# Optimization experiments

Hardware: AMD Instinct MI355X
Metric: run time of the kernel (lower is better)

Reference implementation:

```python
import jax, jax.numpy as jnp
import numpy as np

B, D, HID = 32768, 5, 128
MU, SIGMA = 0.05, 0.2
T_MAX = 1.0


def setup_inputs() -> dict:
    key = jax.random.key(0)
    ks = jax.random.split(key, 5)
    t = T_MAX * jax.random.uniform(ks[0], (B, 1), jnp.float32)          # t in [t0, T]
    x = 0.5 + 2.0 * jax.random.uniform(ks[1], (B, D), jnp.float32)      # domain sampling as in fit()
    Win = jax.random.normal(ks[2], (D + 1, HID), jnp.float32) / np.float32(np.sqrt(D + 1))
    b_in = jnp.zeros((HID,), jnp.float32)
    # 3 DGM layers x 4 gates (Z, G, R, H), each Linear(d+1+HID, HID)
    Wg = jax.random.normal(ks[3], (3, 4, D + 1 + HID, HID), jnp.float32) / np.float32(np.sqrt(D + 1 + HID))
    bg = jnp.zeros((3, 4, HID), jnp.float32)
    Wout = jax.random.normal(ks[4], (HID, 1), jnp.float32) / np.float32(np.sqrt(HID))
    bout = jnp.zeros((1,), jnp.float32)
    return {"t": t, "x": x, "Win": Win, "b_in": b_in, "Wg": Wg, "bg": bg,
            "Wout": Wout, "bout": bout}


def _net(Win, b_in, Wg, bg, Wout, bout, t, x):
    """Net_DGM forward: input layer + 3 gated DGM layers + output layer. u: [B,1]."""
    tx = jnp.concatenate([t, x], axis=1)                 # [B, D+1]
    S = jnp.tanh(tx @ Win + b_in)                        # [B, HID]
    for i in range(3):                                   # fixed small layer loop
        xS = jnp.concatenate([tx, S], axis=1)            # [B, D+1+HID]
        Z = jnp.tanh(xS @ Wg[i, 0] + bg[i, 0])
        G = jnp.tanh(xS @ Wg[i, 1] + bg[i, 1])
        R = jnp.tanh(xS @ Wg[i, 2] + bg[i, 2])
        H = jnp.tanh(jnp.concatenate([tx, S * R], axis=1) @ Wg[i, 3] + bg[i, 3])
        S = (1.0 - G) * H + Z * S
    return S @ Wout + bout                               # [B, 1]


def reference(t, x, Win, b_in, Wg, bg, Wout, bout):
    """Black-Scholes PDE residual: u_t + mu*x.grad_x(u) + 0.5*sigma^2*Lap(u) - mu*u."""
    def u_sum(tt, xx):
        return _net(Win, b_in, Wg, bg, Wout, bout, tt, xx).sum()

    u = _net(Win, b_in, Wg, bg, Wout, bout, t, x)        # [B,1]
    grad_t, grad_x = jax.grad(u_sum, argnums=(0, 1))(t, x)  # [B,1], [B,D]

    # Hessian diagonal via forward-over-reverse (replaces torch's per-dim grad loop)
    gx = lambda xx: jax.grad(u_sum, argnums=1)(t, xx)    # [B,D] -> [B,D]

    def hvp(e):                                          # e: [D] unit vector
        return jax.jvp(gx, (x,), (jnp.broadcast_to(e, x.shape),))[1]  # [B,D]

    Hd = jax.vmap(hvp)(jnp.eye(D, dtype=x.dtype))        # [D, B, D]
    lap = jnp.einsum('ibi->b', Hd)[:, None]              # sum of Hessian diagonal, [B,1]

    drift = jnp.sum(MU * jax.lax.stop_gradient(x) * grad_x, axis=1, keepdims=True)
    pde = grad_t + drift + 0.5 * SIGMA ** 2 * lap - MU * u
    return pde
```

## Files before the change

### kernel.cpp

```cpp
#include <hip/hip_runtime.h>
#include <math.h>


namespace {
constexpr int HID_  = 128;
constexpr int NCH   = 12;
constexpr int ASTR  = 16;
constexpr int SPB   = 4;
constexpr float MU_   = 0.05f;
constexpr float HSIG2 = 0.5f * 0.2f * 0.2f;
}

__global__ __launch_bounds__(64 * SPB, 3)
void dgm_pde(const float* __restrict__ t,
             const float* __restrict__ x,
             const float* __restrict__ Win,
             const float* __restrict__ b_in,
             const float* __restrict__ Wg,
             const float* __restrict__ bg,
             const float* __restrict__ Wout,
             const float* __restrict__ bout,
             float* __restrict__ out)
{
    __shared__ __align__(16) float Abuf[SPB][HID_][ASTR];
    const int wv = threadIdx.x >> 6;
    const int l  = threadIdx.x & 63;
    const int samp = blockIdx.x * SPB + wv;
    float (*A)[ASTR] = Abuf[wv];
    const int j0 = 2 * l;

    float tx[6];
    tx[0] = t[samp];
    #pragma unroll
    for (int m = 1; m < 6; ++m) tx[m] = x[samp * 5 + m - 1];

    float S0[NCH], S1[NCH];
    {
        float w0[6], w1[6];
        #pragma unroll
        for (int m = 0; m < 6; ++m) {
            const float2 ww = *reinterpret_cast<const float2*>(Win + m * HID_ + j0);
            w0[m] = ww.x; w1[m] = ww.y;
        }
        const float2 bb = *reinterpret_cast<const float2*>(b_in + j0);
        float p0 = bb.x, p1 = bb.y;
        #pragma unroll
        for (int m = 0; m < 6; ++m) { p0 = fmaf(tx[m], w0[m], p0); p1 = fmaf(tx[m], w1[m], p1); }
        const float v0 = tanhf(p0), v1 = tanhf(p1);
        const float t20 = 1.f - v0 * v0, t21 = 1.f - v1 * v1;
        S0[0] = v0; S1[0] = v1;
        #pragma unroll
        for (int m = 0; m < 6; ++m) { S0[1 + m] = t20 * w0[m]; S1[1 + m] = t21 * w1[m]; }
        #pragma unroll
        for (int k = 1; k <= 5; ++k) {
            S0[6 + k] = -2.f * v0 * t20 * w0[k] * w0[k];
            S1[6 + k] = -2.f * v1 * t21 * w1[k] * w1[k];
        }
    }

    auto storeA = [&](const float* a0, const float* a1) {
        #pragma unroll
        for (int c = 0; c < NCH; c += 4) {
            *reinterpret_cast<float4*>(&A[j0][c])     = make_float4(a0[c], a0[c+1], a0[c+2], a0[c+3]);
            *reinterpret_cast<float4*>(&A[j0 + 1][c]) = make_float4(a1[c], a1[c+1], a1[c+2], a1[c+3]);
        }
    };
    auto matmul = [&](const float* __restrict__ Wgt, const float* __restrict__ bgt,
                      float* acc0, float* acc1) {
        #pragma unroll
        for (int c = 0; c < NCH; ++c) { acc0[c] = 0.f; acc1[c] = 0.f; }
        const float2 bb = *reinterpret_cast<const float2*>(bgt + j0);
        acc0[0] = bb.x; acc1[0] = bb.y;
        #pragma unroll
        for (int m = 0; m < 6; ++m) {
            const float2 w = *reinterpret_cast<const float2*>(Wgt + m * HID_ + j0);
            acc0[0] = fmaf(tx[m], w.x, acc0[0]);
            acc1[0] = fmaf(tx[m], w.y, acc1[0]);
            acc0[1 + m] += w.x;
            acc1[1 + m] += w.y;
        }
        #pragma unroll 2
        for (int h = 0; h < HID_; ++h) {
            const float2 w = *reinterpret_cast<const float2*>(Wgt + (6 + h) * HID_ + j0);
            const float4* A4 = reinterpret_cast<const float4*>(A[h]);
            const float4 a0 = A4[0], a1 = A4[1], a2 = A4[2];
            const float av[12] = {a0.x, a0.y, a0.z, a0.w,
                                  a1.x, a1.y, a1.z, a1.w,
                                  a2.x, a2.y, a2.z, a2.w};
            #pragma unroll
            for (int c = 0; c < NCH; ++c) {
                acc0[c] = fmaf(av[c], w.x, acc0[c]);
                acc1[c] = fmaf(av[c], w.y, acc1[c]);
            }
        }
    };
    auto act = [&](float* a) {
        const float v  = tanhf(a[0]);
        const float t2 = 1.f - v * v;
        #pragma unroll
        for (int k = 1; k <= 5; ++k) a[6 + k] = t2 * a[6 + k] - 2.f * v * t2 * a[1 + k] * a[1 + k];
        #pragma unroll
        for (int m = 0; m < 6; ++m) a[1 + m] = t2 * a[1 + m];
        a[0] = v;
    };

    storeA(S0, S1);
    __syncthreads();

    float Z0[NCH], Z1[NCH], G0[NCH], G1[NCH], R0[NCH], R1[NCH];
    constexpr int GSTride = 134 * HID_;
    #pragma unroll 1
    for (int layer = 0; layer < 3; ++layer) {
        const float* WL = Wg + (size_t)layer * 4 * GSTride;
        const float* bL = bg + layer * 4 * HID_;

        matmul(WL + 0 * GSTride, bL + 0 * HID_, Z0, Z1); act(Z0); act(Z1);
        matmul(WL + 1 * GSTride, bL + 1 * HID_, G0, G1); act(G0); act(G1);
        matmul(WL + 2 * GSTride, bL + 2 * HID_, R0, R1); act(R0); act(R1);

        #pragma unroll
        for (int k = 1; k <= 5; ++k) {
            R0[6+k] = S0[6+k]*R0[0] + 2.f*S0[1+k]*R0[1+k] + S0[0]*R0[6+k];
            R1[6+k] = S1[6+k]*R1[0] + 2.f*S1[1+k]*R1[1+k] + S1[0]*R1[6+k];
        }
        #pragma unroll
        for (int m = 0; m < 6; ++m) {
            R0[1+m] = S0[1+m]*R0[0] + S0[0]*R0[1+m];
            R1[1+m] = S1[1+m]*R1[0] + S1[0]*R1[1+m];
        }
        R0[0] = S0[0]*R0[0];
        R1[0] = S1[0]*R1[0];

        __syncthreads();
        storeA(R0, R1);
        __syncthreads();

        matmul(WL + 3 * GSTride, bL + 3 * HID_, R0, R1); act(R0); act(R1);

        #pragma unroll
        for (int k = 1; k <= 5; ++k) {
            S0[6+k] = (1.f - G0[0])*R0[6+k] - G0[6+k]*R0[0] - 2.f*G0[1+k]*R0[1+k]
                    + Z0[6+k]*S0[0] + 2.f*Z0[1+k]*S0[1+k] + Z0[0]*S0[6+k];
            S1[6+k] = (1.f - G1[0])*R1[6+k] - G1[6+k]*R1[0] - 2.f*G1[1+k]*R1[1+k]
                    + Z1[6+k]*S1[0] + 2.f*Z1[1+k]*S1[1+k] + Z1[0]*S1[6+k];
        }
        #pragma unroll
        for (int m = 0; m < 6; ++m) {
            S0[1+m] = (1.f - G0[0])*R0[1+m] - G0[1+m]*R0[0] + Z0[1+m]*S0[0] + Z0[0]*S0[1+m];
            S1[1+m] = (1.f - G1[0])*R1[1+m] - G1[1+m]*R1[0] + Z1[1+m]*S1[0] + Z1[0]*S1[1+m];
        }
        S0[0] = (1.f - G0[0])*R0[0] + Z0[0]*S0[0];
        S1[0] = (1.f - G1[0])*R1[0] + Z1[0]*S1[0];

        __syncthreads();
        storeA(S0, S1);
        __syncthreads();
    }

    float comb0 = S0[1] - MU_ * S0[0];
    float comb1 = S1[1] - MU_ * S1[0];
    #pragma unroll
    for (int k = 1; k <= 5; ++k) {
        comb0 += MU_ * tx[k] * S0[1 + k] + HSIG2 * S0[6 + k];
        comb1 += MU_ * tx[k] * S1[1 + k] + HSIG2 * S1[6 + k];
    }
    const float2 wo = *reinterpret_cast<const float2*>(Wout + j0);
    float part = comb0 * wo.x + comb1 * wo.y;
    #pragma unroll
    for (int off = 32; off > 0; off >>= 1) part += __shfl_xor(part, off, 64);
    if (l == 0) out[samp] = part - MU_ * bout[0];
}

extern "C" void kernel_launch(void* const* d_in, const int* in_sizes, int n_in,
                              void* d_out, int out_size, void* d_ws, size_t ws_size,
                              hipStream_t stream)
{
    const float* t    = (const float*)d_in[0];
    const float* x    = (const float*)d_in[1];
    const float* Win  = (const float*)d_in[2];
    const float* b_in = (const float*)d_in[3];
    const float* Wg   = (const float*)d_in[4];
    const float* bg   = (const float*)d_in[5];
    const float* Wout = (const float*)d_in[6];
    const float* bout = (const float*)d_in[7];
    float* out = (float*)d_out;

    const int nB = in_sizes[0];
    dgm_pde<<<nB / SPB, 64 * SPB, 0, stream>>>(t, x, Win, b_in, Wg, bg, Wout, bout, out);
}
```

Baseline: 2.680 ms.

## Use one-wave blocks, double-buffer S/P tiles, reorder gates and software-pipeline the matmul loads

Switches from four samples per 256-thread block to one sample per 64-thread block, with separate shared buffers for S and S*R. Gate evaluation is reordered so Z and G no longer need to live across the H matmul, which cuts register pressure. The inner matmul is hand software-pipelined, prefetching LDS rows and weight pairs two steps ahead. The intent is to hide load latency and raise occupancy, at the cost of more blocks and per-block overhead.

```diff
diff --git a/kernel.cpp b/kernel.cpp
--- a/kernel.cpp
+++ b/kernel.cpp
@@ -3,15 +3,36 @@
 
 
 namespace {
-constexpr int HID_  = 128;
-constexpr int NCH   = 12;
-constexpr int ASTR  = 16;
-constexpr int SPB   = 4;
+constexpr int HID_ = 128;
+constexpr int NCH  = 12;
+constexpr int ASTR = 16;
 constexpr float MU_   = 0.05f;
 constexpr float HSIG2 = 0.5f * 0.2f * 0.2f;
 }
 
-__global__ __launch_bounds__(64 * SPB, 3)
+#define LOADA(AB, h, A0, A1, A2) do {                                     \
+    const float4* _A4 = reinterpret_cast<const float4*>((AB)[(h)]);       \
+    A0 = _A4[0]; A1 = _A4[1]; A2 = _A4[2]; } while (0)
+
+#define LOADW(h, Wv) do {                                                 \
+    Wv = *reinterpret_cast<const float2*>(Wb + (size_t)(h) * HID_); } while (0)
+
+#define FMA12(A0, A1, A2, Wv) do {                                        \
+    acc0[0]  = fmaf((A0).x, (Wv).x, acc0[0]);  acc1[0]  = fmaf((A0).x, (Wv).y, acc1[0]);  \
+    acc0[1]  = fmaf((A0).y, (Wv).x, acc0[1]);  acc1[1]  = fmaf((A0).y, (Wv).y, acc1[1]);  \
+    acc0[2]  = fmaf((A0).z, (Wv).x, acc0[2]);  acc1[2]  = fmaf((A0).z, (Wv).y, acc1[2]);  \
+    acc0[3]  = fmaf((A0).w, (Wv).x, acc0[3]);  acc1[3]  = fmaf((A0).w, (Wv).y, acc1[3]);  \
+    acc0[4]  = fmaf((A1).x, (Wv).x, acc0[4]);  acc1[4]  = fmaf((A1).x, (Wv).y, acc1[4]);  \
+    acc0[5]  = fmaf((A1).y, (Wv).x, acc0[5]);  acc1[5]  = fmaf((A1).y, (Wv).y, acc1[5]);  \
+    acc0[6]  = fmaf((A1).z, (Wv).x, acc0[6]);  acc1[6]  = fmaf((A1).z, (Wv).y, acc1[6]);  \
+    acc0[7]  = fmaf((A1).w, (Wv).x, acc0[7]);  acc1[7]  = fmaf((A1).w, (Wv).y, acc1[7]);  \
+    acc0[8]  = fmaf((A2).x, (Wv).x, acc0[8]);  acc1[8]  = fmaf((A2).x, (Wv).y, acc1[8]);  \
+    acc0[9]  = fmaf((A2).y, (Wv).x, acc0[9]);  acc1[9]  = fmaf((A2).y, (Wv).y, acc1[9]);  \
+    acc0[10] = fmaf((A2).z, (Wv).x, acc0[10]); acc1[10] = fmaf((A2).z, (Wv).y, acc1[10]); \
+    acc0[11] = fmaf((A2).w, (Wv).x, acc0[11]); acc1[11] = fmaf((A2).w, (Wv).y, acc1[11]); \
+} while (0)
+
+__global__ __launch_bounds__(64, 3)
 void dgm_pde(const float* __restrict__ t,
              const float* __restrict__ x,
              const float* __restrict__ Win,
@@ -22,12 +43,11 @@
              const float* __restrict__ bout,
              float* __restrict__ out)
 {
-    __shared__ __align__(16) float Abuf[SPB][HID_][ASTR];
-    const int wv = threadIdx.x >> 6;
-    const int l  = threadIdx.x & 63;
-    const int samp = blockIdx.x * SPB + wv;
-    float (*A)[ASTR] = Abuf[wv];
-    const int j0 = 2 * l;
+    __shared__ __align__(16) float A_S[HID_][ASTR];
+    __shared__ __align__(16) float A_P[HID_][ASTR];
+    const int l    = threadIdx.x;
+    const int samp = blockIdx.x;
+    const int j0   = 2 * l;
 
     float tx[6];
     tx[0] = t[samp];
@@ -58,41 +78,55 @@
         }
     }
 
-    auto storeA = [&](const float* a0, const float* a1) {
+    auto storeJ = [&](float (*AB)[ASTR], const float* a0, const float* a1) {
         #pragma unroll
         for (int c = 0; c < NCH; c += 4) {
-            *reinterpret_cast<float4*>(&A[j0][c])     = make_float4(a0[c], a0[c+1], a0[c+2], a0[c+3]);
-            *reinterpret_cast<float4*>(&A[j0 + 1][c]) = make_float4(a1[c], a1[c+1], a1[c+2], a1[c+3]);
-        }
-    };
-    auto matmul = [&](const float* __restrict__ Wgt, const float* __restrict__ bgt,
-                      float* acc0, float* acc1) {
-        #pragma unroll
-        for (int c = 0; c < NCH; ++c) { acc0[c] = 0.f; acc1[c] = 0.f; }
-        const float2 bb = *reinterpret_cast<const float2*>(bgt + j0);
-        acc0[0] = bb.x; acc1[0] = bb.y;
+            *reinterpret_cast<float4*>(&AB[j0][c])     = make_float4(a0[c], a0[c+1], a0[c+2], a0[c+3]);
+            *reinterpret_cast<float4*>(&AB[j0 + 1][c]) = make_float4(a1[c], a1[c+1], a1[c+2], a1[c+3]);
+        }
+    };
+    auto matmul = [&](const float (*Ab)[ASTR],
+                      const float* __restrict__ Wgt, const float* __restrict__ bgt,
+                      float* __restrict__ acc0, float* __restrict__ acc1) {
+        #pragma unroll
+        for (int c = 1; c < NCH; ++c) { acc0[c] = 0.f; acc1[c] = 0.f; }
+        {
+            const float2 bb = *reinterpret_cast<const float2*>(bgt + j0);
+            acc0[0] = bb.x; acc1[0] = bb.y;
+        }
         #pragma unroll
         for (int m = 0; m < 6; ++m) {
-            const float2 w = *reinterpret_cast<const float2*>(Wgt + m * HID_ + j0);
-            acc0[0] = fmaf(tx[m], w.x, acc0[0]);
-            acc1[0] = fmaf(tx[m], w.y, acc1[0]);
-            acc0[1 + m] += w.x;
-            acc1[1 + m] += w.y;
-        }
-        #pragma unroll 2
-        for (int h = 0; h < HID_; ++h) {
-            const float2 w = *reinterpret_cast<const float2*>(Wgt + (6 + h) * HID_ + j0);
-            const float4* A4 = reinterpret_cast<const float4*>(A[h]);
-            const float4 a0 = A4[0], a1 = A4[1], a2 = A4[2];
-            const float av[12] = {a0.x, a0.y, a0.z, a0.w,
-                                  a1.x, a1.y, a1.z, a1.w,
-                                  a2.x, a2.y, a2.z, a2.w};
-            #pragma unroll
-            for (int c = 0; c < NCH; ++c) {
-                acc0[c] = fmaf(av[c], w.x, acc0[c]);
-                acc1[c] = fmaf(av[c], w.y, acc1[c]);
-            }
-        }
+            const float2 wh = *reinterpret_cast<const float2*>(Wgt + m * HID_ + j0);
+            acc0[0] = fmaf(tx[m], wh.x, acc0[0]);
+            acc1[0] = fmaf(tx[m], wh.y, acc1[0]);
+            acc0[1 + m] += wh.x; acc1[1 + m] += wh.y;
+        }
+        const float* Wb = Wgt + 6 * HID_ + j0;
+        float4 pa0, pa1, pa2, qa0, qa1, qa2;
+        float2 wr0, wr1, wr2, wr3;
+        LOADW(0, wr0); LOADW(1, wr1); LOADW(2, wr2); LOADW(3, wr3);
+        LOADA(Ab, 0, pa0, pa1, pa2);
+        LOADA(Ab, 1, qa0, qa1, qa2);
+        #pragma unroll 4
+        for (int h = 0; h + 5 < HID_; h += 2) {
+            float4 na0, na1, na2, ma0, ma1, ma2;
+            float2 t0, t1;
+            LOADA(Ab, h + 2, na0, na1, na2);
+            LOADA(Ab, h + 3, ma0, ma1, ma2);
+            LOADW(h + 4, t0); LOADW(h + 5, t1);
+            FMA12(pa0, pa1, pa2, wr0);
+            FMA12(qa0, qa1, qa2, wr1);
+            pa0 = na0; pa1 = na1; pa2 = na2;
+            qa0 = ma0; qa1 = ma1; qa2 = ma2;
+            wr0 = wr2; wr1 = wr3; wr2 = t0; wr3 = t1;
+        }
+        float4 na0, na1, na2, ma0, ma1, ma2;
+        LOADA(Ab, 126, na0, na1, na2);
+        LOADA(Ab, 127, ma0, ma1, ma2);
+        FMA12(pa0, pa1, pa2, wr0);
+        FMA12(qa0, qa1, qa2, wr1);
+        FMA12(na0, na1, na2, wr2);
+        FMA12(ma0, ma1, ma2, wr3);
     };
     auto act = [&](float* a) {
         const float v  = tanhf(a[0]);
@@ -103,57 +137,58 @@
         for (int m = 0; m < 6; ++m) a[1 + m] = t2 * a[1 + m];
         a[0] = v;
     };
-
-    storeA(S0, S1);
+    auto prodS = [&](const float* s, float* a) {
+        #pragma unroll
+        for (int k = 1; k <= 5; ++k)
+            a[6+k] = s[6+k]*a[0] + 2.f*s[1+k]*a[1+k] + s[0]*a[6+k];
+        #pragma unroll
+        for (int m = 0; m < 6; ++m)
+            a[1+m] = s[1+m]*a[0] + s[0]*a[1+m];
+        a[0] = s[0]*a[0];
+    };
+
+    storeJ(A_S, S0, S1);
     __syncthreads();
 
-    float Z0[NCH], Z1[NCH], G0[NCH], G1[NCH], R0[NCH], R1[NCH];
+    float Zc0[NCH], Zc1[NCH], Rc0[NCH], Rc1[NCH];
     constexpr int GSTride = 134 * HID_;
     #pragma unroll 1
     for (int layer = 0; layer < 3; ++layer) {
         const float* WL = Wg + (size_t)layer * 4 * GSTride;
         const float* bL = bg + layer * 4 * HID_;
 
-        matmul(WL + 0 * GSTride, bL + 0 * HID_, Z0, Z1); act(Z0); act(Z1);
-        matmul(WL + 1 * GSTride, bL + 1 * HID_, G0, G1); act(G0); act(G1);
-        matmul(WL + 2 * GSTride, bL + 2 * HID_, R0, R1); act(R0); act(R1);
+        matmul(A_S, WL + 2 * GSTride, bL + 2 * HID_, Rc0, Rc1);
+        act(Rc0); act(Rc1);
+        prodS(S0, Rc0); prodS(S1, Rc1);
+        __syncthreads();
+        storeJ(A_P, Rc0, Rc1);
+        __syncthreads();
+
+        matmul(A_P, WL + 3 * GSTride, bL + 3 * HID_, Rc0, Rc1);
+        act(Rc0); act(Rc1);
+
+        matmul(A_S, WL + 0 * GSTride, bL + 0 * HID_, Zc0, Zc1);
+        act(Zc0); act(Zc1);
+        prodS(S0, Zc0); prodS(S1, Zc1);
+
+        matmul(A_S, WL + 1 * GSTride, bL + 1 * HID_, S0, S1);
+        act(S0); act(S1);
 
         #pragma unroll
         for (int k = 1; k <= 5; ++k) {
-            R0[6+k] = S0[6+k]*R0[0] + 2.f*S0[1+k]*R0[1+k] + S0[0]*R0[6+k];
-            R1[6+k] = S1[6+k]*R1[0] + 2.f*S1[1+k]*R1[1+k] + S1[0]*R1[6+k];
+            S0[6+k] = Zc0[6+k] + (1.f - S0[0])*Rc0[6+k] - S0[6+k]*Rc0[0] - 2.f*S0[1+k]*Rc0[1+k];
+            S1[6+k] = Zc1[6+k] + (1.f - S1[0])*Rc1[6+k] - S1[6+k]*Rc1[0] - 2.f*S1[1+k]*Rc1[1+k];
         }
         #pragma unroll
         for (int m = 0; m < 6; ++m) {
-            R0[1+m] = S0[1+m]*R0[0] + S0[0]*R0[1+m];
-            R1[1+m] = S1[1+m]*R1[0] + S1[0]*R1[1+m];
-        }
-        R0[0] = S0[0]*R0[0];
-        R1[0] = S1[0]*R1[0];
-
-        __syncthreads();
-        storeA(R0, R1);
-        __syncthreads();
-
-        matmul(WL + 3 * GSTride, bL + 3 * HID_, R0, R1); act(R0); act(R1);
-
-        #pragma unroll
-        for (int k = 1; k <= 5; ++k) {
-            S0[6+k] = (1.f - G0[0])*R0[6+k] - G0[6+k]*R0[0] - 2.f*G0[1+k]*R0[1+k]
-                    + Z0[6+k]*S0[0] + 2.f*Z0[1+k]*S0[1+k] + Z0[0]*S0[6+k];
-            S1[6+k] = (1.f - G1[0])*R1[6+k] - G1[6+k]*R1[0] - 2.f*G1[1+k]*R1[1+k]
-                    + Z1[6+k]*S1[0] + 2.f*Z1[1+k]*S1[1+k] + Z1[0]*S1[6+k];
-        }
-        #pragma unroll
-        for (int m = 0; m < 6; ++m) {
-            S0[1+m] = (1.f - G0[0])*R0[1+m] - G0[1+m]*R0[0] + Z0[1+m]*S0[0] + Z0[0]*S0[1+m];
-            S1[1+m] = (1.f - G1[0])*R1[1+m] - G1[1+m]*R1[0] + Z1[1+m]*S1[0] + Z1[0]*S1[1+m];
-        }
-        S0[0] = (1.f - G0[0])*R0[0] + Z0[0]*S0[0];
-        S1[0] = (1.f - G1[0])*R1[0] + Z1[0]*S1[0];
-
-        __syncthreads();
-        storeA(S0, S1);
+            S0[1+m] = Zc0[1+m] + (1.f - S0[0])*Rc0[1+m] - S0[1+m]*Rc0[0];
+            S1[1+m] = Zc1[1+m] + (1.f - S1[0])*Rc1[1+m] - S1[1+m]*Rc1[0];
+        }
+        S0[0] = Zc0[0] + (1.f - S0[0])*Rc0[0];
+        S1[0] = Zc1[0] + (1.f - S1[0])*Rc1[0];
+
+        __syncthreads();
+        storeJ(A_S, S0, S1);
         __syncthreads();
     }
 
@@ -186,5 +221,5 @@
     float* out = (float*)d_out;
 
     const int nB = in_sizes[0];
-    dgm_pde<<<nB / SPB, 64 * SPB, 0, stream>>>(t, x, Win, b_in, Wg, bg, Wout, bout, out);
+    dgm_pde<<<nB, 64, 0, stream>>>(t, x, Win, b_in, Wg, bg, Wout, bout, out);
 }
```

Result: slower. 4.274 ms (+59.5%).
